# Kernel optimization log

Hardware: AMD Instinct MI355X
Metric: run time of the kernel (lower is better)

The kernel has to match this reference:

```python
import jax, jax.numpy as jnp
import numpy as np

TOP_K = 2  # cfg.MODEL.MOE.TOP_K


def setup_inputs() -> dict:
    key = jax.random.key(0)
    ks = jax.random.split(key, 5)
    bs, L, d_in, d_out, E = 32, 1024, 768, 256, 8
    return {
        "x": jax.random.normal(ks[0], (bs, L, d_in), dtype=jnp.float32),
        "gate_W": jax.random.normal(ks[1], (d_in, E), dtype=jnp.float32) * (1.0 / np.sqrt(d_in)),
        "gate_b": jax.random.normal(ks[2], (E,), dtype=jnp.float32) * 0.01,
        "expert_W": jax.random.normal(ks[3], (E, d_in, d_out), dtype=jnp.float32) * (1.0 / np.sqrt(d_in)),
        "expert_b": jax.random.normal(ks[4], (E, d_out), dtype=jnp.float32) * 0.01,
    }


def reference(x, gate_W, gate_b, expert_W, expert_b):
    # Gate: (bs, L, E) softmax over experts, then top-k routing weights.
    gate_logits = jnp.einsum("bli,ie->ble", x, gate_W) + gate_b
    gate_weights = jax.nn.softmax(gate_logits, axis=-1)
    topk_vals, topk_idx = jax.lax.top_k(gate_weights, TOP_K)  # (bs, L, K)

    # Dense all-expert projection (E is small), then gather the selected ones.
    # all_out: (bs, L, E, d_out)
    all_out = jnp.einsum("bli,eio->bleo", x, expert_W) + expert_b

    # Select top-k expert outputs per token: (bs, L, K, d_out)
    sel = jnp.take_along_axis(all_out, topk_idx[..., None], axis=2)

    # Weighted combine over the K routed experts -> (bs, L, d_out)
    output = jnp.sum(sel * topk_vals[..., None], axis=2)
    return output
```

## Files before the change

### kernel.cpp

```cpp
#include <hip/hip_runtime.h>
#include <hip/hip_bf16.h>
#include <stdint.h>

#define T_TOKENS 32768
#define D_IN     768
#define D_OUT    256
#define N_EXP    8
#define S_TOT    (T_TOKENS*2)
#define S_PAD    66560
#define NKB      24
#define NT2      12

typedef __attribute__((ext_vector_type(8))) short bf16x8;
typedef __attribute__((ext_vector_type(4))) float f32x4;

__device__ __forceinline__ unsigned short f2bf(float f) {
    unsigned u = __float_as_uint(f);
    return (unsigned short)((u + 0x7FFFu + ((u >> 16) & 1u)) >> 16);
}
__device__ __forceinline__ unsigned pack_bf2(float a, float b) {
    return (unsigned)f2bf(a) | ((unsigned)f2bf(b) << 16);
}

__device__ __forceinline__ void async16(void* lds, const void* g) {
    __builtin_amdgcn_global_load_lds(
        (const __attribute__((address_space(1))) unsigned int*)g,
        (__attribute__((address_space(3))) unsigned int*)lds, 16, 0, 0);
}

__global__ __launch_bounds__(256) void convw_kernel(
        const float* __restrict__ W, unsigned short* __restrict__ WTb,
        int* __restrict__ zero16) {
    if (blockIdx.x == 0 && threadIdx.x < 16) zero16[threadIdx.x] = 0;
    int eb_ = blockIdx.x;
    int n = threadIdx.x;
    const float* src = W + ((size_t)(eb_ / NKB) * D_IN + (eb_ % NKB) * 32) * 256 + n;
    unsigned pk[16];
    #pragma unroll
    for (int j = 0; j < 16; j++)
        pk[j] = pack_bf2(src[(2*j) * 256], src[(2*j+1) * 256]);
    unsigned* dst = (unsigned*)(WTb + ((size_t)eb_ * 256 + n) * 32);
    #pragma unroll
    for (int j = 0; j < 16; j++) dst[j] = pk[j];
}

__global__ __launch_bounds__(256) void gate_fused_kernel(
        const float* __restrict__ x, const float* __restrict__ gW,
        const float* __restrict__ gb, unsigned short* __restrict__ xbf,
        float* __restrict__ topk_w, int* __restrict__ topk_e,
        int* __restrict__ counts) {
    __shared__ float4 gws4[1536];
    __shared__ int h8[8];
    int tid = threadIdx.x;
    if (tid < 8) h8[tid] = 0;
    #pragma unroll
    for (int i = 0; i < 6; ++i) {
        int f = tid + i * 256;
        gws4[f ^ ((f >> 3) & 7)] = *(const float4*)(gW + f * 4);
    }
    int t0 = blockIdx.x * 32;
    int tt = tid >> 3, qq = tid & 7;
    int t  = t0 + tt;
    const float*    xrow  = x   + (size_t)t * D_IN + qq * 4;
    unsigned short* xbrow = xbf + (size_t)t * D_IN + qq * 4;
    float acc[8] = {0,0,0,0,0,0,0,0};
    __syncthreads();
    #pragma unroll 4
    for (int kk = 0; kk < 24; ++kk) {
        float4 v = *(const float4*)(xrow + kk * 32);
        uint2 p; p.x = pack_bf2(v.x, v.y); p.y = pack_bf2(v.z, v.w);
        *(uint2*)(xbrow + kk * 32) = p;
        float vv[4] = {v.x, v.y, v.z, v.w};
        #pragma unroll
        for (int j = 0; j < 4; ++j) {
            int i0 = 8 * qq + 64 * kk + 2 * j;
            float4 g0 = gws4[i0 ^ qq];
            float4 g1 = gws4[(i0 + 1) ^ qq];
            float xv = vv[j];
            acc[0] += xv * g0.x; acc[1] += xv * g0.y;
            acc[2] += xv * g0.z; acc[3] += xv * g0.w;
            acc[4] += xv * g1.x; acc[5] += xv * g1.y;
            acc[6] += xv * g1.z; acc[7] += xv * g1.w;
        }
    }
    #pragma unroll
    for (int e = 0; e < 8; ++e) {
        acc[e] += __shfl_xor(acc[e], 1);
        acc[e] += __shfl_xor(acc[e], 2);
        acc[e] += __shfl_xor(acc[e], 4);
    }
    if (qq == 0) {
        float mx = -1e30f;
        #pragma unroll
        for (int e = 0; e < 8; ++e) { acc[e] += gb[e]; mx = fmaxf(mx, acc[e]); }
        float w[8], s = 0.f;
        #pragma unroll
        for (int e = 0; e < 8; ++e) { w[e] = expf(acc[e] - mx); s += w[e]; }
        float inv = 1.0f / s;
        int e0 = 0; float b0 = -1.f;
        #pragma unroll
        for (int e = 0; e < 8; ++e) if (w[e] > b0) { b0 = w[e]; e0 = e; }
        int e1 = 0; float b1 = -1.f;
        #pragma unroll
        for (int e = 0; e < 8; ++e) if (e != e0 && w[e] > b1) { b1 = w[e]; e1 = e; }
        topk_w[t*2]   = b0 * inv;
        topk_w[t*2+1] = b1 * inv;
        topk_e[t*2]   = e0;
        topk_e[t*2+1] = e1;
        atomicAdd(&h8[e0], 1); atomicAdd(&h8[e1], 1);
    }
    __syncthreads();
    if (tid < 8) atomicAdd(&counts[tid], h8[tid]);
}

__global__ void scatter_kernel(const int* __restrict__ topk_e, const float* __restrict__ topk_w,
                               const int* __restrict__ counts, int* __restrict__ cursors,
                               int* __restrict__ slot_token, float* __restrict__ slot_w,
                               int* __restrict__ inv_slot) {
    int offs[9]; offs[0] = 0;
    #pragma unroll
    for (int e = 0; e < 8; e++) offs[e+1] = offs[e] + ((counts[e] + 127) & ~127);
    if (blockIdx.x == 0) {
        #pragma unroll
        for (int e = 0; e < 8; e++) {
            int start = offs[e] + counts[e];
            for (int i = start + threadIdx.x; i < offs[e+1]; i += 256) slot_w[i] = 0.f;
        }
    }
    __shared__ int hcnt[8], hbase[8];
    if (threadIdx.x < 8) hcnt[threadIdx.x] = 0;
    __syncthreads();
    int idx[4], ee[4], lr[4];
    int base = blockIdx.x * 256 * 4 + threadIdx.x;
    #pragma unroll
    for (int j = 0; j < 4; j++) {
        idx[j] = base + j * 256;
        ee[j]  = topk_e[idx[j]];
        lr[j]  = atomicAdd(&hcnt[ee[j]], 1);
    }
    __syncthreads();
    if (threadIdx.x < 8) hbase[threadIdx.x] = atomicAdd(&cursors[threadIdx.x], hcnt[threadIdx.x]);
    __syncthreads();
    #pragma unroll
    for (int j = 0; j < 4; j++) {
        int slot = offs[ee[j]] + hbase[ee[j]] + lr[j];
        slot_token[slot] = idx[j] >> 1;
        slot_w[slot]     = topk_w[idx[j]];
        inv_slot[idx[j]] = slot;
    }
}

template<bool ROUTED>
__global__ __launch_bounds__(512, 4) void moe_gemm_kernel(
        const unsigned short* __restrict__ xbf, const unsigned short* __restrict__ WTb,
        const float* __restrict__ eb, const int* __restrict__ counts,
        const int* __restrict__ slot_token, const float* __restrict__ slot_w,
        float* __restrict__ dst) {
    __shared__ unsigned short A_lds[3][2][128 * 32];

    int lbid = (blockIdx.x & 7) * ((int)gridDim.x >> 3) + (blockIdx.x >> 3);

    int offs[9]; offs[0] = 0;
    #pragma unroll
    for (int e = 0; e < 8; e++) offs[e+1] = offs[e] + ((counts[e] + 127) & ~127);
    int row0 = lbid * 128;
    if (row0 >= offs[8]) return;
    int expert = 0;
    #pragma unroll
    for (int e = 0; e < 8; e++) if (row0 >= offs[e]) expert = e;

    int tid  = threadIdx.x;
    int wave = tid >> 6, lane = tid & 63;
    int lrow = lane & 15, lquad = lane >> 4;
    int wn = wave;

    int ar = tid >> 2, ap = tid & 3;
    int alc = (ap - (ar >> 1)) & 3;
    int tok = slot_token[row0 + ar];
    tok = (tok < 0 || tok >= T_TOKENS) ? 0 : tok;
    const unsigned short* asrc = xbf + (size_t)tok * D_IN + alc * 8;

    const unsigned short* bptr = WTb + (size_t)expert * NKB * 8192
                                     + (wn * 32 + lrow) * 32 + lquad * 8;

    int a_off[8];
    #pragma unroll
    for (int m = 0; m < 8; m++) {
        int r = m * 16 + lrow;
        a_off[m] = r * 32 + ((lquad + (r >> 1)) & 3) * 8;
    }

    f32x4 acc[8][2];
    #pragma unroll
    for (int m = 0; m < 8; m++)
        #pragma unroll
        for (int q = 0; q < 2; q++) acc[m][q] = (f32x4){0,0,0,0};

    auto bload = [&](int kb, bf16x8 (&b)[2]) {
        const unsigned short* bp = bptr + (size_t)kb * 8192;
        #pragma unroll
        for (int q = 0; q < 2; q++) b[q] = *(const bf16x8*)(bp + q * 512);
    };
    auto stageA = [&](int st, int t2) {
        async16(&A_lds[st][0][tid * 8], asrc + (2 * t2) * 32);
        async16(&A_lds[st][1][tid * 8], asrc + (2 * t2 + 1) * 32);
    };
    auto half = [&](const unsigned short* base, bf16x8 (&b)[2]) {
        #pragma unroll
        for (int g = 0; g < 2; ++g) {
            bf16x8 a[4];
            #pragma unroll
            for (int m = 0; m < 4; ++m) a[m] = *(const bf16x8*)&base[a_off[g*4+m]];
            __builtin_amdgcn_s_setprio(1);
            #pragma unroll
            for (int q = 0; q < 2; ++q)
                #pragma unroll
                for (int m = 0; m < 4; ++m)
                    acc[g*4+m][q] = __builtin_amdgcn_mfma_f32_16x16x32_bf16(
                        a[m], b[q], acc[g*4+m][q], 0, 0, 0);
            __builtin_amdgcn_s_setprio(0);
        }
    };

    stageA(0, 0);
    stageA(1, 1);
    __builtin_amdgcn_sched_barrier(0);
    bf16x8 bEv[2];
    bload(0, bEv);

    for (int t = 0; t < NT2; ++t) {
        if (t == 0 || t == NT2 - 1) asm volatile("s_waitcnt vmcnt(4)" ::: "memory");
        else                        asm volatile("s_waitcnt vmcnt(6)" ::: "memory");
        asm volatile("s_barrier" ::: "memory");
        bf16x8 bOdd[2];
        bload(2 * t + 1, bOdd);
        if (t + 2 < NT2) stageA((t + 2) % 3, t + 2);
        half(&A_lds[t % 3][0][0], bEv);
        bf16x8 bEvN[2];
        if (t + 1 < NT2) bload(2 * t + 2, bEvN);
        half(&A_lds[t % 3][1][0], bOdd);
        if (t + 1 < NT2) { bEv[0] = bEvN[0]; bEv[1] = bEvN[1]; }
    }

    float bias_q[2];
    #pragma unroll
    for (int q = 0; q < 2; q++)
        bias_q[q] = eb[expert * D_OUT + wn * 32 + q * 16 + lrow];
    #pragma unroll
    for (int m = 0; m < 8; m++) {
        #pragma unroll
        for (int r = 0; r < 4; r++) {
            int slot = row0 + m * 16 + lquad * 4 + r;
            if constexpr (ROUTED) {
                float* drow = dst + (size_t)slot * D_OUT + wn * 32;
                #pragma unroll
                for (int q = 0; q < 2; q++)
                    drow[q * 16 + lrow] = acc[m][q][r] + bias_q[q];
            } else {
                int tk = slot_token[slot];
                float wgt = slot_w[slot];
                if (wgt != 0.f) {
                    #pragma unroll
                    for (int q = 0; q < 2; q++)
                        atomicAdd(dst + (size_t)tk * D_OUT + wn * 32 + q * 16 + lrow,
                                  wgt * (acc[m][q][r] + bias_q[q]));
                }
            }
        }
    }
}

__global__ void combine_kernel(const float* __restrict__ routed, const int* __restrict__ inv_slot,
                               const float* __restrict__ topk_w, float* __restrict__ out) {
    int flat = blockIdx.x * 256 + threadIdx.x;
    int t = flat >> 6, c = (flat & 63) * 4;
    int   s0 = inv_slot[t*2], s1 = inv_slot[t*2+1];
    float w0 = topk_w[t*2],   w1 = topk_w[t*2+1];
    float4 r0 = *(const float4*)(routed + (size_t)s0 * D_OUT + c);
    float4 r1 = *(const float4*)(routed + (size_t)s1 * D_OUT + c);
    float4 o;
    o.x = w0*r0.x + w1*r1.x; o.y = w0*r0.y + w1*r1.y;
    o.z = w0*r0.z + w1*r1.z; o.w = w0*r0.w + w1*r1.w;
    *(float4*)(out + (size_t)t * D_OUT + c) = o;
}

extern "C" void kernel_launch(void* const* d_in, const int* in_sizes, int n_in,
                              void* d_out, int out_size, void* d_ws, size_t ws_size,
                              hipStream_t stream) {
    const float* x  = (const float*)d_in[0];
    const float* gW = (const float*)d_in[1];
    const float* gb = (const float*)d_in[2];
    const float* eW = (const float*)d_in[3];
    const float* eb = (const float*)d_in[4];
    float* out = (float*)d_out;
    char* ws = (char*)d_ws;

    float* topk_w      = (float*)(ws + 0);
    int*   topk_e      = (int*)  (ws + 262144);
    int*   counts      = (int*)  (ws + 524288);
    int*   cursors     = (int*)  (ws + 524320);
    int*   slot_token  = (int*)  (ws + 524416);
    float* slot_w      = (float*)(ws + 790656);
    int*   inv_slot    = (int*)  (ws + 1056896);
    unsigned short* WTb= (unsigned short*)(ws + 7610496);
    unsigned short* xbf= (unsigned short*)(ws + 10756224);
    float* routed      = (float*)(ws + 61087872);
    const size_t NEED_ROUTED = 61087872 + (size_t)S_PAD * D_OUT * 4;
    bool use_routed = (ws_size >= NEED_ROUTED);

    convw_kernel      <<<N_EXP * NKB, 256, 0, stream>>>(eW, WTb, counts);
    gate_fused_kernel <<<T_TOKENS / 32, 256, 0, stream>>>(x, gW, gb, xbf,
                                                          topk_w, topk_e, counts);
    scatter_kernel    <<<S_TOT / (256 * 4), 256, 0, stream>>>(topk_e, topk_w, counts, cursors,
                                                              slot_token, slot_w, inv_slot);
    if (use_routed) {
        moe_gemm_kernel<true><<<S_PAD / 128, 512, 0, stream>>>(xbf, WTb, eb, counts,
                                                               slot_token, slot_w, routed);
        combine_kernel<<<T_TOKENS * D_OUT / 4 / 256, 256, 0, stream>>>(routed, inv_slot,
                                                                       topk_w, out);
    } else {
        hipMemsetAsync(slot_token, 0, 532480, stream);
        hipMemsetAsync(out, 0, (size_t)out_size * sizeof(float), stream);
        moe_gemm_kernel<false><<<S_PAD / 128, 512, 0, stream>>>(xbf, WTb, eb, counts,
                                                                slot_token, slot_w, out);
    }
}
```

Baseline: 244.4 us.

## Restructure gate kernel: split K across waves, LDS transpose, ballot histogram

The gate kernel is rewritten so each block handles 64 tokens, with each of the four waves covering a 192-wide K slice. Each lane stages x through a padded LDS transpose so it owns one token, reads gate weights straight from global/scalar memory, and prefetches the next chunk into registers. Per-wave partial logits are reduced through LDS, and the expert histogram uses wave ballots in place of shared atomics. This is meant to remove the shuffle reductions and the LDS weight preload, and to raise memory-level parallelism on the x read. The costs are extra LDS traffic and a serial tail where only one wave does the softmax and top-k.

```diff
diff --git a/kernel.cpp b/kernel.cpp
--- a/kernel.cpp
+++ b/kernel.cpp
@@ -44,73 +44,86 @@
     for (int j = 0; j < 16; j++) dst[j] = pk[j];
 }
 
-__global__ __launch_bounds__(256) void gate_fused_kernel(
+__global__ __launch_bounds__(256) void gate_v4_kernel(
         const float* __restrict__ x, const float* __restrict__ gW,
         const float* __restrict__ gb, unsigned short* __restrict__ xbf,
         float* __restrict__ topk_w, int* __restrict__ topk_e,
         int* __restrict__ counts) {
-    __shared__ float4 gws4[1536];
-    __shared__ int h8[8];
+    __shared__ float lds[4][2112];
     int tid = threadIdx.x;
-    if (tid < 8) h8[tid] = 0;
-    #pragma unroll
-    for (int i = 0; i < 6; ++i) {
-        int f = tid + i * 256;
-        gws4[f ^ ((f >> 3) & 7)] = *(const float4*)(gW + f * 4);
-    }
-    int t0 = blockIdx.x * 32;
-    int tt = tid >> 3, qq = tid & 7;
-    int t  = t0 + tt;
-    const float*    xrow  = x   + (size_t)t * D_IN + qq * 4;
-    unsigned short* xbrow = xbf + (size_t)t * D_IN + qq * 4;
+    int w = tid >> 6, l = tid & 63;
+    int t0 = blockIdx.x * 64;
+    int kb = w * 192;
+    int ti = l >> 3, kloc = (l & 7) * 4;
+    const float*    xsrc = x   + (size_t)(t0 + ti) * D_IN + kb + kloc;
+    unsigned short* xdst = xbf + (size_t)(t0 + ti) * D_IN + kb + kloc;
+    float* myt = &lds[w][0];
+
+    float4 rv[8];
+    #pragma unroll
+    for (int i = 0; i < 8; ++i)
+        rv[i] = *(const float4*)(xsrc + (size_t)i * 8 * D_IN);
     float acc[8] = {0,0,0,0,0,0,0,0};
+
+    #pragma unroll 1
+    for (int c = 0; c < 6; ++c) {
+        #pragma unroll
+        for (int i = 0; i < 8; ++i) {
+            float4 v = rv[i];
+            *(float4*)&myt[(ti + 8 * i) * 33 + kloc] = v;
+            uint2 p; p.x = pack_bf2(v.x, v.y); p.y = pack_bf2(v.z, v.w);
+            *(uint2*)(xdst + (size_t)i * 8 * D_IN + c * 32) = p;
+        }
+        if (c < 5) {
+            #pragma unroll
+            for (int i = 0; i < 8; ++i)
+                rv[i] = *(const float4*)(xsrc + (size_t)i * 8 * D_IN + (c + 1) * 32);
+        }
+        const float* gWc = gW + (size_t)(kb + c * 32) * 8;
+        #pragma unroll
+        for (int k = 0; k < 32; ++k) {
+            float xv = myt[l * 33 + k];
+            const float* gr = gWc + k * 8;
+            #pragma unroll
+            for (int e = 0; e < 8; ++e) acc[e] = fmaf(xv, gr[e], acc[e]);
+        }
+    }
+    #pragma unroll
+    for (int e = 0; e < 8; ++e) myt[l * 9 + e] = acc[e];
     __syncthreads();
-    #pragma unroll 4
-    for (int kk = 0; kk < 24; ++kk) {
-        float4 v = *(const float4*)(xrow + kk * 32);
-        uint2 p; p.x = pack_bf2(v.x, v.y); p.y = pack_bf2(v.z, v.w);
-        *(uint2*)(xbrow + kk * 32) = p;
-        float vv[4] = {v.x, v.y, v.z, v.w};
-        #pragma unroll
-        for (int j = 0; j < 4; ++j) {
-            int i0 = 8 * qq + 64 * kk + 2 * j;
-            float4 g0 = gws4[i0 ^ qq];
-            float4 g1 = gws4[(i0 + 1) ^ qq];
-            float xv = vv[j];
-            acc[0] += xv * g0.x; acc[1] += xv * g0.y;
-            acc[2] += xv * g0.z; acc[3] += xv * g0.w;
-            acc[4] += xv * g1.x; acc[5] += xv * g1.y;
-            acc[6] += xv * g1.z; acc[7] += xv * g1.w;
-        }
-    }
-    #pragma unroll
-    for (int e = 0; e < 8; ++e) {
-        acc[e] += __shfl_xor(acc[e], 1);
-        acc[e] += __shfl_xor(acc[e], 2);
-        acc[e] += __shfl_xor(acc[e], 4);
-    }
-    if (qq == 0) {
+    if (w == 0) {
+        int t = t0 + l;
+        float s8[8];
+        #pragma unroll
+        for (int e = 0; e < 8; ++e)
+            s8[e] = ((lds[0][l*9+e] + lds[1][l*9+e])
+                   + (lds[2][l*9+e] + lds[3][l*9+e])) + gb[e];
         float mx = -1e30f;
         #pragma unroll
-        for (int e = 0; e < 8; ++e) { acc[e] += gb[e]; mx = fmaxf(mx, acc[e]); }
-        float w[8], s = 0.f;
-        #pragma unroll
-        for (int e = 0; e < 8; ++e) { w[e] = expf(acc[e] - mx); s += w[e]; }
+        for (int e = 0; e < 8; ++e) mx = fmaxf(mx, s8[e]);
+        float pw[8], s = 0.f;
+        #pragma unroll
+        for (int e = 0; e < 8; ++e) { pw[e] = expf(s8[e] - mx); s += pw[e]; }
         float inv = 1.0f / s;
         int e0 = 0; float b0 = -1.f;
         #pragma unroll
-        for (int e = 0; e < 8; ++e) if (w[e] > b0) { b0 = w[e]; e0 = e; }
+        for (int e = 0; e < 8; ++e) if (pw[e] > b0) { b0 = pw[e]; e0 = e; }
         int e1 = 0; float b1 = -1.f;
         #pragma unroll
-        for (int e = 0; e < 8; ++e) if (e != e0 && w[e] > b1) { b1 = w[e]; e1 = e; }
+        for (int e = 0; e < 8; ++e) if (e != e0 && pw[e] > b1) { b1 = pw[e]; e1 = e; }
         topk_w[t*2]   = b0 * inv;
         topk_w[t*2+1] = b1 * inv;
         topk_e[t*2]   = e0;
         topk_e[t*2+1] = e1;
-        atomicAdd(&h8[e0], 1); atomicAdd(&h8[e1], 1);
-    }
-    __syncthreads();
-    if (tid < 8) atomicAdd(&counts[tid], h8[tid]);
+        int my = 0;
+        #pragma unroll
+        for (int e = 0; e < 8; ++e) {
+            unsigned long long m0 = __ballot(e0 == e);
+            unsigned long long m1 = __ballot(e1 == e);
+            if (l == e) my = __popcll(m0) + __popcll(m1);
+        }
+        if (l < 8) atomicAdd(&counts[l], my);
+    }
 }
 
 __global__ void scatter_kernel(const int* __restrict__ topk_e, const float* __restrict__ topk_w,
@@ -308,11 +321,11 @@
     const size_t NEED_ROUTED = 61087872 + (size_t)S_PAD * D_OUT * 4;
     bool use_routed = (ws_size >= NEED_ROUTED);
 
-    convw_kernel      <<<N_EXP * NKB, 256, 0, stream>>>(eW, WTb, counts);
-    gate_fused_kernel <<<T_TOKENS / 32, 256, 0, stream>>>(x, gW, gb, xbf,
-                                                          topk_w, topk_e, counts);
-    scatter_kernel    <<<S_TOT / (256 * 4), 256, 0, stream>>>(topk_e, topk_w, counts, cursors,
-                                                              slot_token, slot_w, inv_slot);
+    convw_kernel   <<<N_EXP * NKB, 256, 0, stream>>>(eW, WTb, counts);
+    gate_v4_kernel <<<T_TOKENS / 64, 256, 0, stream>>>(x, gW, gb, xbf,
+                                                       topk_w, topk_e, counts);
+    scatter_kernel <<<S_TOT / (256 * 4), 256, 0, stream>>>(topk_e, topk_w, counts, cursors,
+                                                           slot_token, slot_w, inv_slot);
     if (use_routed) {
         moe_gemm_kernel<true><<<S_PAD / 128, 512, 0, stream>>>(xbf, WTb, eb, counts,
                                                                slot_token, slot_w, routed);
```

New measurement: 266.0 us. 1.09x slower.
